# Kernel tuning notes

Measured on AMD Instinct MI355X. Metric: run time of the kernel, lower is better.

The kernel has to match this reference:

```python
import jax, jax.numpy as jnp
import numpy as np

FEAT = 64
K = 16
K4 = K // 4
EPS = 1e-5  # BatchNorm eps (inference mode with running stats)


def _conv1x1(x, w, b):
    # x: (B, Cin, N, K), w: (Cout, Cin), b: (Cout,)
    return jnp.einsum('oc,bcnk->bonk', w, x) + b[None, :, None, None]


def _bn(x, g, be, m, v):
    # inference-mode BatchNorm2d over channel axis 1
    inv = g / jnp.sqrt(v + EPS)
    return (x - m[None, :, None, None]) * inv[None, :, None, None] + be[None, :, None, None]


def setup_inputs() -> dict:
    key = jax.random.key(0)
    ks = jax.random.split(key, 20)
    B, N, M = 4, 8192, 8192
    d = {}
    d['original_pts'] = jax.random.normal(ks[0], (B, 3, M), dtype=jnp.float32)
    d['query_pts'] = jax.random.normal(ks[1], (B, 3, N), dtype=jnp.float32)
    d['local_feat'] = jax.random.normal(ks[2], (B, FEAT, M), dtype=jnp.float32)
    # mlp_0: Conv2D(3, FEAT) with BN + ReLU
    d['w0'] = jax.random.normal(ks[3], (FEAT, 3), dtype=jnp.float32) * 0.2
    d['b0'] = jax.random.normal(ks[4], (FEAT,), dtype=jnp.float32) * 0.01
    d['g0'] = 1.0 + 0.1 * jax.random.normal(ks[5], (FEAT,), dtype=jnp.float32)
    d['be0'] = 0.01 * jax.random.normal(ks[6], (FEAT,), dtype=jnp.float32)
    d['m0'] = 0.01 * jax.random.normal(ks[7], (FEAT,), dtype=jnp.float32)
    d['v0'] = jax.random.uniform(ks[8], (FEAT,), dtype=jnp.float32, minval=0.5, maxval=1.5)
    # mlp_1: Conv2D(FEAT, FEAT) with BN + ReLU
    d['w1'] = jax.random.normal(ks[9], (FEAT, FEAT), dtype=jnp.float32) * 0.1
    d['b1'] = jax.random.normal(ks[10], (FEAT,), dtype=jnp.float32) * 0.01
    d['g1'] = 1.0 + 0.1 * jax.random.normal(ks[11], (FEAT,), dtype=jnp.float32)
    d['be1'] = 0.01 * jax.random.normal(ks[12], (FEAT,), dtype=jnp.float32)
    d['m1'] = 0.01 * jax.random.normal(ks[13], (FEAT,), dtype=jnp.float32)
    d['v1'] = jax.random.uniform(ks[14], (FEAT,), dtype=jnp.float32, minval=0.5, maxval=1.5)
    # mlp_2: Conv2D(2*FEAT, 1), no BN, no ReLU
    d['w2'] = jax.random.normal(ks[15], (1, 2 * FEAT), dtype=jnp.float32) * 0.1
    d['b2'] = jax.random.normal(ks[16], (1,), dtype=jnp.float32) * 0.01
    return d


def reference(original_pts, query_pts, local_feat,
              w0, b0, g0, be0, m0, v0,
              w1, b1, g1, be1, m1, v1,
              w2, b2):
    B, _, N = query_pts.shape
    # --- KNN: squared distances (B, N, M), take K smallest ---
    q2 = jnp.sum(query_pts ** 2, axis=1)          # (B, N)
    o2 = jnp.sum(original_pts ** 2, axis=1)       # (B, M)
    cross = jnp.einsum('bcn,bcm->bnm', query_pts, original_pts)
    d2 = q2[:, :, None] + o2[:, None, :] - 2.0 * cross
    _, knn_idx = jax.lax.top_k(-d2, K)            # (B, N, K)

    # gather neighbor coords: (B, 3, N, K)
    knn_pts = jax.vmap(lambda pts, idx: pts[:, idx])(original_pts, knn_idx)
    # gather local features for first K//4 neighbors: (B, FEAT, N, K4)
    patch_feat = jax.vmap(lambda f, idx: f[:, idx])(local_feat, knn_idx[:, :, :K4])

    relative_pts = knn_pts - query_pts[:, :, :, None]  # (B, 3, N, K)
    feat0 = jax.nn.relu(_bn(_conv1x1(relative_pts, w0, b0), g0, be0, m0, v0))  # (B, F, N, K)
    feat_g = jnp.max(feat0, axis=3, keepdims=True)                              # (B, F, N, 1)
    relative_feat = jax.nn.relu(_bn(_conv1x1(feat0, w1, b1), g1, be1, m1, v1))[:, :, :, :K4]
    feat2 = jnp.concatenate(
        [relative_feat, jnp.broadcast_to(feat_g, (B, FEAT, N, K4))], axis=1)    # (B, 2F, N, K4)
    weight = jax.nn.sigmoid(_conv1x1(feat2, w2, b2))                            # (B, 1, N, K4)
    query_feat = (1.0 - weight) * relative_feat + weight * patch_feat
    return jnp.sum(query_feat, axis=-1)  # (B, FEAT, N)
```

## Files before the change

### kernel.cpp

```cpp
#include <hip/hip_runtime.h>
#include <cstdint>

#define M_PTS 8192
#define N_QRY 8192
#define BATCH 4

typedef unsigned long long ull;

__device__ __forceinline__ float d2_exact(float qx, float qy, float qz, float q2, float4 p) {
#pragma clang fp contract(off)
  float dot = (qx * p.x + qy * p.y) + qz * p.z;
  return (q2 + p.w) - 2.0f * dot;
}

__device__ __forceinline__ unsigned flipf(float d) {
  unsigned u = __float_as_uint(d);
  return u ^ ((unsigned)((int)u >> 31) | 0x80000000u);
}

__device__ __forceinline__ int lane_prefix(unsigned long long m) {
  return __builtin_amdgcn_mbcnt_hi((unsigned)(m >> 32),
         __builtin_amdgcn_mbcnt_lo((unsigned)m, 0));
}

__device__ __forceinline__ void ld_lds16(const float4* g, float4* l) {
  __builtin_amdgcn_global_load_lds((const __attribute__((address_space(1))) void*)g,
                                   (__attribute__((address_space(3))) void*)l, 16, 0, 0);
}

__device__ __forceinline__ float tau16(float mn) {
  float lo = mn, hi = mn;
#pragma unroll
  for (int j = 1; j < 64; j <<= 1) {
    lo = fminf(lo, __shfl_xor(lo, j));
    hi = fmaxf(hi, __shfl_xor(hi, j));
  }
#pragma unroll
  for (int it = 0; it < 10; it++) {
    float mid = 0.5f * (lo + hi);
    int cnt = __popcll(__ballot(mn <= mid));
    if (cnt >= 16) hi = mid; else lo = mid;
  }
  return hi;
}

__device__ __forceinline__ ull bsort64(ull v, int lane) {
#pragma unroll
  for (int k = 2; k <= 64; k <<= 1) {
#pragma unroll
    for (int j = k >> 1; j >= 1; j >>= 1) {
      ull o = __shfl_xor(v, j);
      bool keepmin = (((lane & k) == 0) == ((lane & j) == 0));
      ull lo = v < o ? v : o;
      ull hi = v < o ? o : v;
      v = keepmin ? lo : hi;
    }
  }
  return v;
}

__global__ void prep_kernel(const float* __restrict__ original_pts,
                            const float* __restrict__ query_pts,
                            const float* __restrict__ lf,
                            float4* __restrict__ pp, float4* __restrict__ qp,
                            float* __restrict__ lfT) {
#pragma clang fp contract(off)
  const int bid = blockIdx.x;
  if (bid < 256) {
    const float* src = (bid < 128) ? original_pts : query_pts;
    float4* dst = (bid < 128) ? pp : qp;
    int i = (bid & 127) * 256 + threadIdx.x;
    int b = i >> 13, m = i & (M_PTS - 1);
    const float* s = src + (size_t)b * 3 * M_PTS;
    float x = s[m], y = s[M_PTS + m], z = s[2 * M_PTS + m];
    float ss = (x * x + y * y) + z * z;
    dst[i] = make_float4(x, y, z, ss);
    return;
  }
  __shared__ float tile[64][65];
  int vbid = bid - 256;
  int bb = vbid >> 7;
  int m0 = (vbid & 127) << 6;
  int tm = threadIdx.x & 63;
  int tc = threadIdx.x >> 6;
  const float* src = lf + (size_t)bb * 64 * M_PTS;
#pragma unroll
  for (int i = 0; i < 16; i++) {
    int ch = i * 4 + tc;
    tile[ch][tm] = src[(size_t)ch * M_PTS + m0 + tm];
  }
  __syncthreads();
  float* dst = lfT + ((size_t)bb * M_PTS + m0) * 64;
#pragma unroll
  for (int i = 0; i < 16; i++) {
    int mm = i * 4 + tc;
    dst[(size_t)mm * 64 + tm] = tile[tm][mm];
  }
}

__global__ void __launch_bounds__(512) fused_kernel(
    const float4* __restrict__ pp, const float4* __restrict__ qp,
    const float* __restrict__ lfT,
    const float* __restrict__ w0, const float* __restrict__ b0,
    const float* __restrict__ g0, const float* __restrict__ be0,
    const float* __restrict__ m0, const float* __restrict__ v0,
    const float* __restrict__ w1, const float* __restrict__ b1,
    const float* __restrict__ g1, const float* __restrict__ be1,
    const float* __restrict__ m1, const float* __restrict__ v1,
    const float* __restrict__ w2, const float* __restrict__ b2,
    float* __restrict__ out) {
  __shared__ __align__(16) char smem[31232];
  __shared__ int sknn[16][16];
  const int tid = threadIdx.x;
  const int lane = tid & 63;
  const int wave = tid >> 6;
  const int gq0 = blockIdx.x * 16;
  const int qa = gq0 + wave * 2;
  const int b = qa >> 13;
  const float4* pb = pp + ((size_t)b << 13);

  {
    ull (*cbuf)[96] = (ull(*)[96])(smem + 16384);

    const float4 A4 = qp[qa];
    const float4 B4 = qp[qa + 1];
    const float axA = -2.0f * A4.x, ayA = -2.0f * A4.y, azA = -2.0f * A4.z;
    const float axB = -2.0f * B4.x, ayB = -2.0f * B4.y, azB = -2.0f * B4.z;

    int cntA = 0, cntB = 0;
    unsigned* cqA = (unsigned*)cbuf[wave * 2 + 0];
    unsigned* cqB = (unsigned*)cbuf[wave * 2 + 1];

    float mnA = 3.402823466e38f, mnB = 3.402823466e38f;
    float tauA = 0.0f, tauB = 0.0f;

    auto bufp = [&](int d) -> float4* {
      return (float4*)(smem + ((size_t)d << 13));
    };

    auto stage = [&](int d, int s) {
      const float4* g = pb + s * 512 + wave * 64 + lane;
      ld_lds16(g, bufp(d) + wave * 64);
    };

    auto minpass = [&](const float4* sp) {
#pragma unroll
      for (int j = 0; j < 8; j++) {
        float4 p = sp[j * 64 + lane];
        mnA = fminf(mnA, __builtin_fmaf(axA, p.x, __builtin_fmaf(ayA, p.y,
                         __builtin_fmaf(azA, p.z, p.w))));
        mnB = fminf(mnB, __builtin_fmaf(axB, p.x, __builtin_fmaf(ayB, p.y,
                         __builtin_fmaf(azB, p.z, p.w))));
      }
    };

    auto collect = [&](float e, float tau, unsigned* cq, int& cnt, unsigned idx) {
      bool pred = e <= tau;
      unsigned long long mask = __ballot(pred);
      if (mask) {
        int pos = cnt + lane_prefix(mask);
        if (pred && pos < 192) cq[pos] = idx;
        cnt += __popcll(mask);
      }
    };

    auto fused = [&](const float4* sp, unsigned base) {
#pragma unroll
      for (int j = 0; j < 8; j++) {
        float4 p = sp[j * 64 + lane];
        float ea = __builtin_fmaf(axA, p.x, __builtin_fmaf(ayA, p.y,
                   __builtin_fmaf(azA, p.z, p.w)));
        float eb = __builtin_fmaf(axB, p.x, __builtin_fmaf(ayB, p.y,
                   __builtin_fmaf(azB, p.z, p.w)));
        mnA = fminf(mnA, ea);
        mnB = fminf(mnB, eb);
        unsigned idx = base + j * 64 + lane;
        collect(ea, tauA, cqA, cntA, idx);
        collect(eb, tauB, cqB, cntB, idx);
      }
    };

    stage(0, 0);
    __syncthreads();
    stage(1, 1);
    minpass(bufp(0));
    __syncthreads();
    minpass(bufp(1));
    tauA = tau16(mnA) + 0.01f;
    tauB = tau16(mnB) + 0.01f;
    fused(bufp(0), 0);
    fused(bufp(1), 512);
    __syncthreads();
    stage(0, 2);
    __syncthreads();

    for (int s = 2; s < 16; ++s) {
      if (s < 15) stage((s + 1) & 1, s + 1);
      fused(bufp(s & 1), (unsigned)(s * 512));
      if (s == 3 || s == 7 || s == 11) {
        tauA = fminf(tauA, tau16(mnA) + 0.01f);
        tauB = fminf(tauB, tau16(mnB) + 0.01f);
      }
      __syncthreads();
    }

    auto finalize = [&](ull* cb, int cnt, int* srow,
                        float qx, float qy, float qz, float q2) {
      unsigned* cu = (unsigned*)cb;
      int E = cnt < 192 ? cnt : 192;
      unsigned i0 = (lane < E) ? cu[lane] : 0u;
      unsigned i1 = (lane + 64 < E) ? cu[lane + 64] : 0u;
      unsigned i2 = (lane + 128 < E) ? cu[lane + 128] : 0u;
      float4 p0 = pb[i0];
      float4 p1 = pb[i1];
      float4 p2 = pb[i2];
      ull k0 = ~0ull, k1 = ~0ull, k2 = ~0ull;
      if (lane < E)
        k0 = ((ull)flipf(d2_exact(qx, qy, qz, q2, p0)) << 32) | i0;
      if (lane + 64 < E)
        k1 = ((ull)flipf(d2_exact(qx, qy, qz, q2, p1)) << 32) | i1;
      if (lane + 128 < E)
        k2 = ((ull)flipf(d2_exact(qx, qy, qz, q2, p2)) << 32) | i2;
      ull ml = k0 < k1 ? k0 : k1;
      if (k2 < ml) ml = k2;
      ull T = __shfl(bsort64(ml, lane), 15);
      int c2 = 0;
      {
        bool pr = k0 <= T; ull m = __ballot(pr);
        int pos = c2 + lane_prefix(m);
        if (pr) cb[pos] = k0;
        c2 += __popcll(m);
      }
      {
        bool pr = k1 <= T; ull m = __ballot(pr);
        int pos = c2 + lane_prefix(m);
        if (pr) cb[pos] = k1;
        c2 += __popcll(m);
      }
      {
        bool pr = k2 <= T; ull m = __ballot(pr);
        int pos = c2 + lane_prefix(m);
        if (pr) cb[pos] = k2;
        c2 += __popcll(m);
      }
      ull kk = (lane < c2) ? cb[lane] : ~0ull;
      ull fin = bsort64(kk, lane);
      if (lane < 16) srow[lane] = (int)(unsigned)fin;
    };

    finalize(cbuf[wave * 2 + 0], cntA, sknn[wave * 2 + 0], A4.x, A4.y, A4.z, A4.w);
    finalize(cbuf[wave * 2 + 1], cntB, sknn[wave * 2 + 1], B4.x, B4.y, B4.z, B4.w);
  }

  __syncthreads();

  float (*w1T)[65]    = (float(*)[65])smem;
  float4 (*relbuf)[16] = (float4(*)[16])(smem + 16640);
  float4 (*f0v)[64]   = (float4(*)[64])(smem + 18688);
  float (*outbuf)[17] = (float(*)[17])(smem + 26880);

  {
    const float4* w1f4 = (const float4*)w1;
#pragma unroll
    for (int k = 0; k < 2; k++) {
      int linear4 = tid + k * 512;
      int c = linear4 >> 4;
      int c2 = (linear4 & 15) * 4;
      float4 t = w1f4[linear4];
      w1T[c2 + 0][c] = t.x;
      w1T[c2 + 1][c] = t.y;
      w1T[c2 + 2][c] = t.z;
      w1T[c2 + 3][c] = t.w;
    }
  }

  const float inv0 = g0[lane] / sqrtf(v0[lane] + 1e-5f);
  const float w00 = w0[lane * 3 + 0] * inv0;
  const float w01 = w0[lane * 3 + 1] * inv0;
  const float w02 = w0[lane * 3 + 2] * inv0;
  const float bb0 = (b0[lane] - m0[lane]) * inv0 + be0[lane];
  const float inv1 = g1[lane] / sqrtf(v1[lane] + 1e-5f);
  const float bb1 = (b1[lane] - m1[lane]) * inv1 + be1[lane];

  const float w2a = w2[lane], w2b = w2[64 + lane];
  const float bias2 = b2[0];
  const float* lfb = lfT + (((size_t)b << 13)) * 64;

  __syncthreads();

  for (int qi = 0; qi < 2; qi++) {
    const int gq = qa + qi;
    const float4 q4 = qp[gq];
    int nk = sknn[wave * 2 + qi][lane & 15];
    float4 pk = pb[nk];
    int i0 = __shfl(nk, 0), i1 = __shfl(nk, 1), i2 = __shfl(nk, 2), i3 = __shfl(nk, 3);
    float p0 = lfb[(size_t)i0 * 64 + lane];
    float p1 = lfb[(size_t)i1 * 64 + lane];
    float p2 = lfb[(size_t)i2 * 64 + lane];
    float p3 = lfb[(size_t)i3 * 64 + lane];

    if (lane < 16)
      relbuf[wave][lane] = make_float4(pk.x - q4.x, pk.y - q4.y, pk.z - q4.z, 0.0f);

    float g = 0.0f, f0 = 0, f1 = 0, f2 = 0, f3 = 0;
#pragma unroll
    for (int k = 0; k < 16; k++) {
      float4 r = relbuf[wave][k];
      float y = fmaxf(0.0f, w00 * r.x + w01 * r.y + w02 * r.z + bb0);
      g = fmaxf(g, y);
      if (k == 0) f0 = y; else if (k == 1) f1 = y;
      else if (k == 2) f2 = y; else if (k == 3) f3 = y;
    }
    f0v[wave][lane] = make_float4(f0, f1, f2, f3);

    float a0 = 0, a1 = 0, a2 = 0, a3 = 0;
#pragma unroll
    for (int c2 = 0; c2 < 64; c2++) {
      float w = w1T[c2][lane];
      float4 fb = f0v[wave][c2];
      a0 = fmaf(w, fb.x, a0); a1 = fmaf(w, fb.y, a1);
      a2 = fmaf(w, fb.z, a2); a3 = fmaf(w, fb.w, a3);
    }
    float r0 = fmaxf(0.0f, fmaf(a0, inv1, bb1));
    float r1 = fmaxf(0.0f, fmaf(a1, inv1, bb1));
    float r2 = fmaxf(0.0f, fmaf(a2, inv1, bb1));
    float r3 = fmaxf(0.0f, fmaf(a3, inv1, bb1));

    float s0 = w2a * r0, s1 = w2a * r1, s2 = w2a * r2, s3 = w2a * r3, tg = w2b * g;
#pragma unroll
    for (int j = 1; j < 64; j <<= 1) {
      s0 += __shfl_xor(s0, j);
      s1 += __shfl_xor(s1, j);
      s2 += __shfl_xor(s2, j);
      s3 += __shfl_xor(s3, j);
      tg += __shfl_xor(tg, j);
    }
    float wk0 = 1.0f / (1.0f + __expf(-(s0 + tg + bias2)));
    float wk1 = 1.0f / (1.0f + __expf(-(s1 + tg + bias2)));
    float wk2 = 1.0f / (1.0f + __expf(-(s2 + tg + bias2)));
    float wk3 = 1.0f / (1.0f + __expf(-(s3 + tg + bias2)));

    float oc = ((1.0f - wk0) * r0 + wk0 * p0)
             + ((1.0f - wk1) * r1 + wk1 * p1)
             + ((1.0f - wk2) * r2 + wk2 * p2)
             + ((1.0f - wk3) * r3 + wk3 * p3);
    outbuf[lane][wave * 2 + qi] = oc;
  }
  __syncthreads();

  if (tid < 256) {
    int c = tid >> 2, j = tid & 3;
    float4 o4 = make_float4(outbuf[c][j * 4 + 0], outbuf[c][j * 4 + 1],
                            outbuf[c][j * 4 + 2], outbuf[c][j * 4 + 3]);
    *(float4*)(out + (((size_t)(b * 64 + c)) << 13) + (gq0 & (N_QRY - 1)) + j * 4) = o4;
  }
}

extern "C" void kernel_launch(void* const* d_in, const int* in_sizes, int n_in,
                              void* d_out, int out_size, void* d_ws, size_t ws_size,
                              hipStream_t stream) {
  (void)in_sizes; (void)n_in; (void)out_size; (void)ws_size;
  const float* original_pts = (const float*)d_in[0];
  const float* query_pts   = (const float*)d_in[1];
  const float* local_feat  = (const float*)d_in[2];
  const float* w0 = (const float*)d_in[3];
  const float* b0 = (const float*)d_in[4];
  const float* g0 = (const float*)d_in[5];
  const float* be0 = (const float*)d_in[6];
  const float* m0 = (const float*)d_in[7];
  const float* v0 = (const float*)d_in[8];
  const float* w1 = (const float*)d_in[9];
  const float* b1 = (const float*)d_in[10];
  const float* g1 = (const float*)d_in[11];
  const float* be1 = (const float*)d_in[12];
  const float* m1 = (const float*)d_in[13];
  const float* v1 = (const float*)d_in[14];
  const float* w2 = (const float*)d_in[15];
  const float* b2 = (const float*)d_in[16];
  float* out = (float*)d_out;

  char* ws = (char*)d_ws;
  float4* pp  = (float4*)(ws);
  float4* qp  = (float4*)(ws + 524288);
  float*  lfT = (float*)(ws + 1048576);

  prep_kernel<<<768, 256, 0, stream>>>(original_pts, query_pts, local_feat,
                                       pp, qp, lfT);
  fused_kernel<<<2048, 512, 0, stream>>>(pp, qp, lfT,
                                         w0, b0, g0, be0, m0, v0,
                                         w1, b1, g1, be1, m1, v1,
                                         w2, b2, out);
}
```

Before: 246.1 us.

## Double block size to 1024 threads with larger shared point tiles

Result: slower. 278.8 us (+13.3%).

```diff
diff --git a/kernel.cpp b/kernel.cpp
--- a/kernel.cpp
+++ b/kernel.cpp
@@ -98,7 +98,7 @@
   }
 }
 
-__global__ void __launch_bounds__(512) fused_kernel(
+__global__ void __launch_bounds__(1024) fused_kernel(
     const float4* __restrict__ pp, const float4* __restrict__ qp,
     const float* __restrict__ lfT,
     const float* __restrict__ w0, const float* __restrict__ b0,
@@ -109,18 +109,18 @@
     const float* __restrict__ m1, const float* __restrict__ v1,
     const float* __restrict__ w2, const float* __restrict__ b2,
     float* __restrict__ out) {
-  __shared__ __align__(16) char smem[31232];
-  __shared__ int sknn[16][16];
+  __shared__ __align__(16) char smem[57344];
+  __shared__ int sknn[32][16];
   const int tid = threadIdx.x;
   const int lane = tid & 63;
   const int wave = tid >> 6;
-  const int gq0 = blockIdx.x * 16;
+  const int gq0 = blockIdx.x * 32;
   const int qa = gq0 + wave * 2;
   const int b = qa >> 13;
   const float4* pb = pp + ((size_t)b << 13);
 
   {
-    ull (*cbuf)[96] = (ull(*)[96])(smem + 16384);
+    unsigned (*cbuf)[192] = (unsigned(*)[192])(smem + 32768);
 
     const float4 A4 = qp[qa];
     const float4 B4 = qp[qa + 1];
@@ -128,24 +128,24 @@
     const float axB = -2.0f * B4.x, ayB = -2.0f * B4.y, azB = -2.0f * B4.z;
 
     int cntA = 0, cntB = 0;
-    unsigned* cqA = (unsigned*)cbuf[wave * 2 + 0];
-    unsigned* cqB = (unsigned*)cbuf[wave * 2 + 1];
+    unsigned* cqA = cbuf[wave * 2 + 0];
+    unsigned* cqB = cbuf[wave * 2 + 1];
 
     float mnA = 3.402823466e38f, mnB = 3.402823466e38f;
     float tauA = 0.0f, tauB = 0.0f;
 
     auto bufp = [&](int d) -> float4* {
-      return (float4*)(smem + ((size_t)d << 13));
+      return (float4*)(smem + ((size_t)d << 14));
     };
 
     auto stage = [&](int d, int s) {
-      const float4* g = pb + s * 512 + wave * 64 + lane;
+      const float4* g = pb + s * 1024 + wave * 64 + lane;
       ld_lds16(g, bufp(d) + wave * 64);
     };
 
     auto minpass = [&](const float4* sp) {
 #pragma unroll
-      for (int j = 0; j < 8; j++) {
+      for (int j = 0; j < 16; j++) {
         float4 p = sp[j * 64 + lane];
         mnA = fminf(mnA, __builtin_fmaf(axA, p.x, __builtin_fmaf(ayA, p.y,
                          __builtin_fmaf(azA, p.z, p.w))));
@@ -166,7 +166,7 @@
 
     auto fused = [&](const float4* sp, unsigned base) {
 #pragma unroll
-      for (int j = 0; j < 8; j++) {
+      for (int j = 0; j < 16; j++) {
         float4 p = sp[j * 64 + lane];
         float ea = __builtin_fmaf(axA, p.x, __builtin_fmaf(ayA, p.y,
                    __builtin_fmaf(azA, p.z, p.w)));
@@ -184,29 +184,25 @@
     __syncthreads();
     stage(1, 1);
     minpass(bufp(0));
-    __syncthreads();
-    minpass(bufp(1));
     tauA = tau16(mnA) + 0.01f;
     tauB = tau16(mnB) + 0.01f;
     fused(bufp(0), 0);
-    fused(bufp(1), 512);
     __syncthreads();
-    stage(0, 2);
-    __syncthreads();
-
-    for (int s = 2; s < 16; ++s) {
-      if (s < 15) stage((s + 1) & 1, s + 1);
-      fused(bufp(s & 1), (unsigned)(s * 512));
-      if (s == 3 || s == 7 || s == 11) {
+
+    for (int s = 1; s < 8; ++s) {
+      if (s < 7) stage((s + 1) & 1, s + 1);
+      fused(bufp(s & 1), (unsigned)(s * 1024));
+      if (s == 1 || s == 3 || s == 5) {
         tauA = fminf(tauA, tau16(mnA) + 0.01f);
         tauB = fminf(tauB, tau16(mnB) + 0.01f);
       }
       __syncthreads();
     }
 
-    auto finalize = [&](ull* cb, int cnt, int* srow,
+    ull* fs = (ull*)(smem + wave * 512);
+
+    auto finalize = [&](unsigned* cu, int cnt, int* srow,
                         float qx, float qy, float qz, float q2) {
-      unsigned* cu = (unsigned*)cb;
       int E = cnt < 192 ? cnt : 192;
       unsigned i0 = (lane < E) ? cu[lane] : 0u;
       unsigned i1 = (lane + 64 < E) ? cu[lane + 64] : 0u;
@@ -228,50 +224,46 @@
       {
         bool pr = k0 <= T; ull m = __ballot(pr);
         int pos = c2 + lane_prefix(m);
-        if (pr) cb[pos] = k0;
+        if (pr) fs[pos] = k0;
         c2 += __popcll(m);
       }
       {
         bool pr = k1 <= T; ull m = __ballot(pr);
         int pos = c2 + lane_prefix(m);
-        if (pr) cb[pos] = k1;
+        if (pr) fs[pos] = k1;
         c2 += __popcll(m);
       }
       {
         bool pr = k2 <= T; ull m = __ballot(pr);
         int pos = c2 + lane_prefix(m);
-        if (pr) cb[pos] = k2;
+        if (pr) fs[pos] = k2;
         c2 += __popcll(m);
       }
-      ull kk = (lane < c2) ? cb[lane] : ~0ull;
+      ull kk = (lane < c2) ? fs[lane] : ~0ull;
       ull fin = bsort64(kk, lane);
       if (lane < 16) srow[lane] = (int)(unsigned)fin;
     };
 
-    finalize(cbuf[wave * 2 + 0], cntA, sknn[wave * 2 + 0], A4.x, A4.y, A4.z, A4.w);
-    finalize(cbuf[wave * 2 + 1], cntB, sknn[wave * 2 + 1], B4.x, B4.y, B4.z, B4.w);
+    finalize(cqA, cntA, sknn[wave * 2 + 0], A4.x, A4.y, A4.z, A4.w);
+    finalize(cqB, cntB, sknn[wave * 2 + 1], B4.x, B4.y, B4.z, B4.w);
   }
 
   __syncthreads();
 
-  float (*w1T)[65]    = (float(*)[65])smem;
+  float (*w1T)[65]     = (float(*)[65])smem;
   float4 (*relbuf)[16] = (float4(*)[16])(smem + 16640);
-  float4 (*f0v)[64]   = (float4(*)[64])(smem + 18688);
-  float (*outbuf)[17] = (float(*)[17])(smem + 26880);
+  float4 (*f0v)[64]    = (float4(*)[64])(smem + 20736);
+  float (*outbuf)[33]  = (float(*)[33])(smem + 37120);
 
   {
     const float4* w1f4 = (const float4*)w1;
-#pragma unroll
-    for (int k = 0; k < 2; k++) {
-      int linear4 = tid + k * 512;
-      int c = linear4 >> 4;
-      int c2 = (linear4 & 15) * 4;
-      float4 t = w1f4[linear4];
-      w1T[c2 + 0][c] = t.x;
-      w1T[c2 + 1][c] = t.y;
-      w1T[c2 + 2][c] = t.z;
-      w1T[c2 + 3][c] = t.w;
-    }
+    int c = tid >> 4;
+    int c2 = (tid & 15) * 4;
+    float4 t = w1f4[tid];
+    w1T[c2 + 0][c] = t.x;
+    w1T[c2 + 1][c] = t.y;
+    w1T[c2 + 2][c] = t.z;
+    w1T[c2 + 3][c] = t.w;
   }
 
   const float inv0 = g0[lane] / sqrtf(v0[lane] + 1e-5f);
@@ -348,8 +340,8 @@
   }
   __syncthreads();
 
-  if (tid < 256) {
-    int c = tid >> 2, j = tid & 3;
+  if (tid < 512) {
+    int c = tid >> 3, j = tid & 7;
     float4 o4 = make_float4(outbuf[c][j * 4 + 0], outbuf[c][j * 4 + 1],
                             outbuf[c][j * 4 + 2], outbuf[c][j * 4 + 3]);
     *(float4*)(out + (((size_t)(b * 64 + c)) << 13) + (gq0 & (N_QRY - 1)) + j * 4) = o4;
@@ -386,8 +378,8 @@
 
   prep_kernel<<<768, 256, 0, stream>>>(original_pts, query_pts, local_feat,
                                        pp, qp, lfT);
-  fused_kernel<<<2048, 512, 0, stream>>>(pp, qp, lfT,
-                                         w0, b0, g0, be0, m0, v0,
-                                         w1, b1, g1, be1, m1, v1,
-                                         w2, b2, out);
-}
+  fused_kernel<<<1024, 1024, 0, stream>>>(pp, qp, lfT,
+                                          w0, b0, g0, be0, m0, v0,
+                                          w1, b1, g1, be1, m1, v1,
+                                          w2, b2, out);
+}
```

## Process four queries per wave to reuse staged point tiles across more queries

Applied to the files above, without the earlier changes.

Measured after the change: 261.0 us. 6.1% more time.

```diff
diff --git a/kernel.cpp b/kernel.cpp
--- a/kernel.cpp
+++ b/kernel.cpp
@@ -109,30 +109,35 @@
     const float* __restrict__ m1, const float* __restrict__ v1,
     const float* __restrict__ w2, const float* __restrict__ b2,
     float* __restrict__ out) {
-  __shared__ __align__(16) char smem[31232];
-  __shared__ int sknn[16][16];
+  __shared__ __align__(16) char smem[40960];
+  __shared__ int sknn[32][16];
   const int tid = threadIdx.x;
   const int lane = tid & 63;
   const int wave = tid >> 6;
-  const int gq0 = blockIdx.x * 16;
-  const int qa = gq0 + wave * 2;
-  const int b = qa >> 13;
+  const int gq0 = blockIdx.x * 32;
+  const int qa = gq0 + wave * 4;
+  const int b = gq0 >> 13;
   const float4* pb = pp + ((size_t)b << 13);
 
   {
-    ull (*cbuf)[96] = (ull(*)[96])(smem + 16384);
-
-    const float4 A4 = qp[qa];
-    const float4 B4 = qp[qa + 1];
-    const float axA = -2.0f * A4.x, ayA = -2.0f * A4.y, azA = -2.0f * A4.z;
-    const float axB = -2.0f * B4.x, ayB = -2.0f * B4.y, azB = -2.0f * B4.z;
-
-    int cntA = 0, cntB = 0;
-    unsigned* cqA = (unsigned*)cbuf[wave * 2 + 0];
-    unsigned* cqB = (unsigned*)cbuf[wave * 2 + 1];
-
-    float mnA = 3.402823466e38f, mnB = 3.402823466e38f;
-    float tauA = 0.0f, tauB = 0.0f;
+    unsigned (*cbuf)[192] = (unsigned(*)[192])(smem + 16384);
+
+    float axA, ayA, azA, axB, ayB, azB, axC, ayC, azC, axD, ayD, azD;
+    {
+      float4 A4 = qp[qa + 0], B4 = qp[qa + 1], C4 = qp[qa + 2], D4 = qp[qa + 3];
+      axA = -2.0f * A4.x; ayA = -2.0f * A4.y; azA = -2.0f * A4.z;
+      axB = -2.0f * B4.x; ayB = -2.0f * B4.y; azB = -2.0f * B4.z;
+      axC = -2.0f * C4.x; ayC = -2.0f * C4.y; azC = -2.0f * C4.z;
+      axD = -2.0f * D4.x; ayD = -2.0f * D4.y; azD = -2.0f * D4.z;
+    }
+    int cntA = 0, cntB = 0, cntC = 0, cntD = 0;
+    unsigned* cqA = cbuf[wave * 4 + 0];
+    unsigned* cqB = cbuf[wave * 4 + 1];
+    unsigned* cqC = cbuf[wave * 4 + 2];
+    unsigned* cqD = cbuf[wave * 4 + 3];
+
+    float mnA = 3.402823466e38f, mnB = mnA, mnC = mnA, mnD = mnA;
+    float tauA = 0.0f, tauB = 0.0f, tauC = 0.0f, tauD = 0.0f;
 
     auto bufp = [&](int d) -> float4* {
       return (float4*)(smem + ((size_t)d << 13));
@@ -143,14 +148,17 @@
       ld_lds16(g, bufp(d) + wave * 64);
     };
 
-    auto minpass = [&](const float4* sp) {
+    auto minpair = [&](const float4* sp,
+                       float ax0, float ay0, float az0,
+                       float ax1, float ay1, float az1,
+                       float& m0r, float& m1r) {
 #pragma unroll
       for (int j = 0; j < 8; j++) {
         float4 p = sp[j * 64 + lane];
-        mnA = fminf(mnA, __builtin_fmaf(axA, p.x, __builtin_fmaf(ayA, p.y,
-                         __builtin_fmaf(azA, p.z, p.w))));
-        mnB = fminf(mnB, __builtin_fmaf(axB, p.x, __builtin_fmaf(ayB, p.y,
-                         __builtin_fmaf(azB, p.z, p.w))));
+        m0r = fminf(m0r, __builtin_fmaf(ax0, p.x, __builtin_fmaf(ay0, p.y,
+                         __builtin_fmaf(az0, p.z, p.w))));
+        m1r = fminf(m1r, __builtin_fmaf(ax1, p.x, __builtin_fmaf(ay1, p.y,
+                         __builtin_fmaf(az1, p.z, p.w))));
       }
     };
 
@@ -164,49 +172,66 @@
       }
     };
 
-    auto fused = [&](const float4* sp, unsigned base) {
+    auto fusedpair = [&](const float4* sp, unsigned base,
+                         float ax0, float ay0, float az0,
+                         float ax1, float ay1, float az1,
+                         float& m0r, float& m1r, float t0, float t1,
+                         unsigned* c0, unsigned* c1, int& n0, int& n1) {
 #pragma unroll
       for (int j = 0; j < 8; j++) {
         float4 p = sp[j * 64 + lane];
-        float ea = __builtin_fmaf(axA, p.x, __builtin_fmaf(ayA, p.y,
-                   __builtin_fmaf(azA, p.z, p.w)));
-        float eb = __builtin_fmaf(axB, p.x, __builtin_fmaf(ayB, p.y,
-                   __builtin_fmaf(azB, p.z, p.w)));
-        mnA = fminf(mnA, ea);
-        mnB = fminf(mnB, eb);
+        float e0 = __builtin_fmaf(ax0, p.x, __builtin_fmaf(ay0, p.y,
+                   __builtin_fmaf(az0, p.z, p.w)));
+        float e1 = __builtin_fmaf(ax1, p.x, __builtin_fmaf(ay1, p.y,
+                   __builtin_fmaf(az1, p.z, p.w)));
+        m0r = fminf(m0r, e0);
+        m1r = fminf(m1r, e1);
         unsigned idx = base + j * 64 + lane;
-        collect(ea, tauA, cqA, cntA, idx);
-        collect(eb, tauB, cqB, cntB, idx);
+        collect(e0, t0, c0, n0, idx);
+        collect(e1, t1, c1, n1, idx);
       }
     };
 
     stage(0, 0);
     __syncthreads();
     stage(1, 1);
-    minpass(bufp(0));
+    minpair(bufp(0), axA, ayA, azA, axB, ayB, azB, mnA, mnB);
+    minpair(bufp(0), axC, ayC, azC, axD, ayD, azD, mnC, mnD);
     __syncthreads();
-    minpass(bufp(1));
+    minpair(bufp(1), axA, ayA, azA, axB, ayB, azB, mnA, mnB);
+    minpair(bufp(1), axC, ayC, azC, axD, ayD, azD, mnC, mnD);
     tauA = tau16(mnA) + 0.01f;
     tauB = tau16(mnB) + 0.01f;
-    fused(bufp(0), 0);
-    fused(bufp(1), 512);
+    tauC = tau16(mnC) + 0.01f;
+    tauD = tau16(mnD) + 0.01f;
+    fusedpair(bufp(0), 0,   axA, ayA, azA, axB, ayB, azB, mnA, mnB, tauA, tauB, cqA, cqB, cntA, cntB);
+    fusedpair(bufp(0), 0,   axC, ayC, azC, axD, ayD, azD, mnC, mnD, tauC, tauD, cqC, cqD, cntC, cntD);
+    fusedpair(bufp(1), 512, axA, ayA, azA, axB, ayB, azB, mnA, mnB, tauA, tauB, cqA, cqB, cntA, cntB);
+    fusedpair(bufp(1), 512, axC, ayC, azC, axD, ayD, azD, mnC, mnD, tauC, tauD, cqC, cqD, cntC, cntD);
     __syncthreads();
     stage(0, 2);
     __syncthreads();
 
     for (int s = 2; s < 16; ++s) {
       if (s < 15) stage((s + 1) & 1, s + 1);
-      fused(bufp(s & 1), (unsigned)(s * 512));
+      const float4* sp = bufp(s & 1);
+      unsigned base = (unsigned)(s * 512);
+      fusedpair(sp, base, axA, ayA, azA, axB, ayB, azB, mnA, mnB, tauA, tauB, cqA, cqB, cntA, cntB);
+      fusedpair(sp, base, axC, ayC, azC, axD, ayD, azD, mnC, mnD, tauC, tauD, cqC, cqD, cntC, cntD);
       if (s == 3 || s == 7 || s == 11) {
         tauA = fminf(tauA, tau16(mnA) + 0.01f);
         tauB = fminf(tauB, tau16(mnB) + 0.01f);
+        tauC = fminf(tauC, tau16(mnC) + 0.01f);
+        tauD = fminf(tauD, tau16(mnD) + 0.01f);
       }
       __syncthreads();
     }
 
-    auto finalize = [&](ull* cb, int cnt, int* srow,
-                        float qx, float qy, float qz, float q2) {
-      unsigned* cu = (unsigned*)cb;
+    ull* fs = (ull*)(smem + wave * 512);
+
+    auto finalize = [&](unsigned* cu, int cnt, int* srow, int gq) {
+      float4 q4 = qp[gq];
+      float qx = q4.x, qy = q4.y, qz = q4.z, q2 = q4.w;
       int E = cnt < 192 ? cnt : 192;
       unsigned i0 = (lane < E) ? cu[lane] : 0u;
       unsigned i1 = (lane + 64 < E) ? cu[lane + 64] : 0u;
@@ -228,36 +253,38 @@
       {
         bool pr = k0 <= T; ull m = __ballot(pr);
         int pos = c2 + lane_prefix(m);
-        if (pr) cb[pos] = k0;
+        if (pr) fs[pos] = k0;
         c2 += __popcll(m);
       }
       {
         bool pr = k1 <= T; ull m = __ballot(pr);
         int pos = c2 + lane_prefix(m);
-        if (pr) cb[pos] = k1;
+        if (pr) fs[pos] = k1;
         c2 += __popcll(m);
       }
       {
         bool pr = k2 <= T; ull m = __ballot(pr);
         int pos = c2 + lane_prefix(m);
-        if (pr) cb[pos] = k2;
+        if (pr) fs[pos] = k2;
         c2 += __popcll(m);
       }
-      ull kk = (lane < c2) ? cb[lane] : ~0ull;
+      ull kk = (lane < c2) ? fs[lane] : ~0ull;
       ull fin = bsort64(kk, lane);
       if (lane < 16) srow[lane] = (int)(unsigned)fin;
     };
 
-    finalize(cbuf[wave * 2 + 0], cntA, sknn[wave * 2 + 0], A4.x, A4.y, A4.z, A4.w);
-    finalize(cbuf[wave * 2 + 1], cntB, sknn[wave * 2 + 1], B4.x, B4.y, B4.z, B4.w);
+    finalize(cqA, cntA, sknn[wave * 4 + 0], qa + 0);
+    finalize(cqB, cntB, sknn[wave * 4 + 1], qa + 1);
+    finalize(cqC, cntC, sknn[wave * 4 + 2], qa + 2);
+    finalize(cqD, cntD, sknn[wave * 4 + 3], qa + 3);
   }
 
   __syncthreads();
 
-  float (*w1T)[65]    = (float(*)[65])smem;
+  float (*w1T)[65]     = (float(*)[65])smem;
   float4 (*relbuf)[16] = (float4(*)[16])(smem + 16640);
-  float4 (*f0v)[64]   = (float4(*)[64])(smem + 18688);
-  float (*outbuf)[17] = (float(*)[17])(smem + 26880);
+  float4 (*f0v)[64]    = (float4(*)[64])(smem + 18688);
+  float (*outbuf)[33]  = (float(*)[33])(smem + 26880);
 
   {
     const float4* w1f4 = (const float4*)w1;
@@ -288,10 +315,10 @@
 
   __syncthreads();
 
-  for (int qi = 0; qi < 2; qi++) {
+  for (int qi = 0; qi < 4; qi++) {
     const int gq = qa + qi;
     const float4 q4 = qp[gq];
-    int nk = sknn[wave * 2 + qi][lane & 15];
+    int nk = sknn[wave * 4 + qi][lane & 15];
     float4 pk = pb[nk];
     int i0 = __shfl(nk, 0), i1 = __shfl(nk, 1), i2 = __shfl(nk, 2), i3 = __shfl(nk, 3);
     float p0 = lfb[(size_t)i0 * 64 + lane];
@@ -344,12 +371,12 @@
              + ((1.0f - wk1) * r1 + wk1 * p1)
              + ((1.0f - wk2) * r2 + wk2 * p2)
              + ((1.0f - wk3) * r3 + wk3 * p3);
-    outbuf[lane][wave * 2 + qi] = oc;
+    outbuf[lane][wave * 4 + qi] = oc;
   }
   __syncthreads();
 
-  if (tid < 256) {
-    int c = tid >> 2, j = tid & 3;
+  {
+    int c = tid >> 3, j = tid & 7;
     float4 o4 = make_float4(outbuf[c][j * 4 + 0], outbuf[c][j * 4 + 1],
                             outbuf[c][j * 4 + 2], outbuf[c][j * 4 + 3]);
     *(float4*)(out + (((size_t)(b * 64 + c)) << 13) + (gq0 & (N_QRY - 1)) + j * 4) = o4;
@@ -386,7 +413,7 @@
 
   prep_kernel<<<768, 256, 0, stream>>>(original_pts, query_pts, local_feat,
                                        pp, qp, lfT);
-  fused_kernel<<<2048, 512, 0, stream>>>(pp, qp, lfT,
+  fused_kernel<<<1024, 512, 0, stream>>>(pp, qp, lfT,
                                          w0, b0, g0, be0, m0, v0,
                                          w1, b1, g1, be1, m1, v1,
                                          w2, b2, out);
```
